# Kernel tuning notes

Hardware: AMD Instinct MI355X
Metric: run time of the kernel (lower is better)

The kernel has to match this reference:

```python
import jax, jax.numpy as jnp
import numpy as np

B, N, M = 16, 4096, 1024
IN_C, OUT_C, D = 6, 128, 64


def _gn(x, w, b, groups, eps=1e-5):
    # GroupNorm over (C//groups, L) per group; x: [B, C, L]
    Bb, C, L = x.shape
    xg = x.reshape(Bb, groups, C // groups, L)
    mu = xg.mean(axis=(2, 3), keepdims=True)
    var = xg.var(axis=(2, 3), keepdims=True)
    xn = ((xg - mu) * jax.lax.rsqrt(var + eps)).reshape(Bb, C, L)
    return xn * w[None, :, None] + b[None, :, None]


def _sa(xq, xkv, xyz_q, xyz_kv, qk_w, v_w, v_b, t_w, t_b, gn_w, gn_b, p_w, pg_w):
    # offset self-attention (PCT SA_Layer), q/k share weights
    pq = jnp.einsum('bcn,dc->bnd', xyz_q, p_w)              # [B,N,D]
    pk = jnp.einsum('bcm,dc->bdm', xyz_kv, pg_w)            # [B,D,M]
    q = jnp.einsum('bcn,dc->bnd', xq, qk_w) + pq            # [B,N,D]
    k = jnp.einsum('bcm,dc->bdm', xkv, qk_w) + pk           # [B,D,M]
    v = jnp.einsum('bcm,dc->bdm', xkv, v_w) + v_b[None, :, None] + pk
    attn = jax.nn.softmax(jnp.einsum('bnd,bdm->bnm', q, k), axis=-1)
    attn = attn / (1e-9 + attn.sum(axis=1, keepdims=True))  # L1 renorm over queries
    x_r = jnp.einsum('bnm,bdm->bnd', attn, v)               # [B,N,D]
    t = jnp.einsum('bnd,od->bon', q - x_r, t_w) + t_b[None, :, None]
    t = jax.nn.relu(_gn(t, gn_w, gn_b, 4))
    return jnp.swapaxes(q, 1, 2) + t                        # [B,D,N]


def _forward(x, x_global, xyz, xyz_global, conv1_w, gn1_w, gn1_b, conv2_w, gn2_w, gn2_b, sa_qk_w, sa_v_w, sa_v_b, sa_trans_w, sa_trans_b, sa_gn_w, sa_gn_b, sa_pos_w, sa_posG_w, fuse_w, fuse_gn_w, fuse_gn_b, convs1_w, convs1_b, gns1_w, gns1_b, convs2_w, convs2_b, gns2_w, gns2_b):
    h = jax.nn.relu(_gn(jnp.einsum('bcn,oc->bon', x, conv1_w), gn1_w, gn1_b, 16))
    hg = jax.nn.relu(_gn(jnp.einsum('bcm,oc->bom', x_global, conv2_w), gn2_w, gn2_b, 16))
    outs = []
    cur = h
    for i in range(4):
        cur = _sa(cur, hg, xyz, xyz_global, sa_qk_w[i], sa_v_w[i], sa_v_b[i],
                  sa_trans_w[i], sa_trans_b[i], sa_gn_w[i], sa_gn_b[i],
                  sa_pos_w[i], sa_posG_w[i])
        outs.append(cur)
    xc = jnp.concatenate(outs, axis=1)                      # [B,4D,N]
    xf = jax.nn.leaky_relu(_gn(jnp.einsum('bcn,oc->bon', xc, fuse_w), fuse_gn_w, fuse_gn_b, 16), 0.2)
    s1 = jax.nn.relu(_gn(jnp.einsum('bcn,oc->bon', xf, convs1_w) + convs1_b[None, :, None], gns1_w, gns1_b, 8))
    # dropout is identity in eval mode
    s2 = jax.nn.relu(_gn(jnp.einsum('bcn,oc->bon', s1, convs2_w) + convs2_b[None, :, None], gns2_w, gns2_b, 4))
    return jnp.swapaxes(s2, 1, 2)                           # [B,N,OUT_C]


def setup_inputs() -> dict:
    ks = jax.random.split(jax.random.key(0), 16)
    f = lambda k, s, sc=0.1: jax.random.normal(k, s, dtype=jnp.float32) * sc
    return {
        'x': f(ks[0], (B, IN_C, N), 1.0),
        'x_global': f(ks[1], (B, 32, M), 1.0),
        'xyz': f(ks[2], (B, 3, N), 1.0),
        'xyz_global': f(ks[3], (B, 3, M), 1.0),
        'conv1_w': f(ks[4], (D, IN_C)),
        'gn1_w': jnp.ones((D,), jnp.float32), 'gn1_b': jnp.zeros((D,), jnp.float32),
        'conv2_w': f(ks[5], (D, 32)),
        'gn2_w': jnp.ones((D,), jnp.float32), 'gn2_b': jnp.zeros((D,), jnp.float32),
        'sa_qk_w': f(ks[6], (4, D, D)),
        'sa_v_w': f(ks[7], (4, D, D)),
        'sa_v_b': jnp.zeros((4, D), jnp.float32),
        'sa_trans_w': f(ks[8], (4, D, D)),
        'sa_trans_b': jnp.zeros((4, D), jnp.float32),
        'sa_gn_w': jnp.ones((4, D), jnp.float32), 'sa_gn_b': jnp.zeros((4, D), jnp.float32),
        'sa_pos_w': f(ks[9], (4, D, 3)),
        'sa_posG_w': f(ks[10], (4, D, 3)),
        'fuse_w': f(ks[11], (2 * D, 4 * D)),
        'fuse_gn_w': jnp.ones((2 * D,), jnp.float32), 'fuse_gn_b': jnp.zeros((2 * D,), jnp.float32),
        'convs1_w': f(ks[12], (512, 2 * D)),
        'convs1_b': jnp.zeros((512,), jnp.float32),
        'gns1_w': jnp.ones((512,), jnp.float32), 'gns1_b': jnp.zeros((512,), jnp.float32),
        'convs2_w': f(ks[13], (OUT_C, 512)),
        'convs2_b': jnp.zeros((OUT_C,), jnp.float32),
        'gns2_w': jnp.ones((OUT_C,), jnp.float32), 'gns2_b': jnp.zeros((OUT_C,), jnp.float32),
    }


def reference(x, x_global, xyz, xyz_global, conv1_w, gn1_w, gn1_b, conv2_w, gn2_w, gn2_b, sa_qk_w, sa_v_w, sa_v_b, sa_trans_w, sa_trans_b, sa_gn_w, sa_gn_b, sa_pos_w, sa_posG_w, fuse_w, fuse_gn_w, fuse_gn_b, convs1_w, convs1_b, gns1_w, gns1_b, convs2_w, convs2_b, gns2_w, gns2_b):
    return _forward(x, x_global, xyz, xyz_global, conv1_w, gn1_w, gn1_b, conv2_w, gn2_w, gn2_b, sa_qk_w, sa_v_w, sa_v_b, sa_trans_w, sa_trans_b, sa_gn_w, sa_gn_b, sa_pos_w, sa_posG_w, fuse_w, fuse_gn_w, fuse_gn_b, convs1_w, convs1_b, gns1_w, gns1_b, convs2_w, convs2_b, gns2_w, gns2_b)
```

## Files before the change

### kernel.cpp

```cpp
#include <hip/hip_runtime.h>
#include <hip/hip_bf16.h>

namespace {

constexpr int BB = 16;
constexpr int NN = 4096;
constexpr int MM = 1024;

using f32x4  = __attribute__((ext_vector_type(4))) float;
using bf16x8 = __attribute__((ext_vector_type(8))) short;

__device__ __forceinline__ float actf(float x, int act) {
    if (act == 1) return fmaxf(x, 0.f);
    if (act == 2) return x >= 0.f ? x : 0.2f * x;
    return x;
}

__device__ __forceinline__ ushort f2bf(float x) {
    __hip_bfloat16 h = __float2bfloat16(x);
    return *reinterpret_cast<ushort*>(&h);
}

__device__ __forceinline__ uint hilo_pack(float x) {
    ushort h = f2bf(x);
    float hf = __uint_as_float(((uint)h) << 16);
    ushort l = f2bf(x - hf);
    return (uint)h | ((uint)l << 16);
}

__device__ __forceinline__ void split8(const uint* d, bf16x8& hi, bf16x8& lo) {
    union { uint u[4]; bf16x8 v; } H, L;
#pragma unroll
    for (int j = 0; j < 4; ++j) {
        H.u[j] = (d[2 * j] & 0xffffu) | (d[2 * j + 1] << 16);
        L.u[j] = (d[2 * j] >> 16) | (d[2 * j + 1] & 0xffff0000u);
    }
    hi = H.v; lo = L.v;
}

__global__ __launch_bounds__(256)
void conv_mfma(const float* __restrict__ X, int C, long x_bs,
               const float* __restrict__ W,
               const float* __restrict__ X2, long x2_bs,
               const float* __restrict__ W2,
               const float* __restrict__ bias,
               float* __restrict__ Y, long y_bs, int L)
{
    __shared__ uint Wp[64 * 33];
    __shared__ uint Xp[128 * 33];
    const int t  = threadIdx.x;
    const int b  = blockIdx.z;
    const int o0 = blockIdx.y * 64;
    const int l0 = blockIdx.x * 128;
    const int w  = t >> 6;
    const int ln = t & 15;
    const int lq = (t >> 4) & 3;
    const int wo = (w & 1) * 32;
    const int wl = (w >> 1) * 64;
    const int sl  = t & 127;
    const int sch = (t >> 7) * 16;

    f32x4 acc[2][4];
#pragma unroll
    for (int i = 0; i < 2; ++i)
#pragma unroll
        for (int j = 0; j < 4; ++j) acc[i][j] = (f32x4){0.f, 0.f, 0.f, 0.f};

    for (int c0 = 0; c0 < C; c0 += 32) {
        __syncthreads();
#pragma unroll
        for (int i = 0; i < 2; ++i) {
            int f = i * 256 + t;
            int r = f >> 3, q4 = (f & 7) * 4;
            float4 wv = *reinterpret_cast<const float4*>(&W[(long)(o0 + r) * C + c0 + q4]);
            Wp[r * 33 + q4 + 0] = hilo_pack(wv.x);
            Wp[r * 33 + q4 + 1] = hilo_pack(wv.y);
            Wp[r * 33 + q4 + 2] = hilo_pack(wv.z);
            Wp[r * 33 + q4 + 3] = hilo_pack(wv.w);
        }
        {
            const float* xc = X + (long)b * x_bs + (long)(c0 + sch) * L + l0 + sl;
            uint tmp[16];
#pragma unroll
            for (int c = 0; c < 16; ++c) tmp[c] = hilo_pack(xc[(long)c * L]);
#pragma unroll
            for (int c4 = 0; c4 < 4; ++c4) {
                uint4 v = make_uint4(tmp[c4 * 4], tmp[c4 * 4 + 1],
                                     tmp[c4 * 4 + 2], tmp[c4 * 4 + 3]);
                *reinterpret_cast<uint4*>(&Xp[sl * 33 + sch + c4 * 4]) = v;
            }
        }
        __syncthreads();

        bf16x8 ahi[2], alo[2];
#pragma unroll
        for (int ot = 0; ot < 2; ++ot) {
            uint d[8];
            *reinterpret_cast<uint4*>(d) =
                *reinterpret_cast<const uint4*>(&Wp[(wo + ot * 16 + ln) * 33 + lq * 8]);
            *reinterpret_cast<uint4*>(d + 4) =
                *reinterpret_cast<const uint4*>(&Wp[(wo + ot * 16 + ln) * 33 + lq * 8 + 4]);
            split8(d, ahi[ot], alo[ot]);
        }
#pragma unroll
        for (int lt = 0; lt < 4; ++lt) {
            uint d[8];
            *reinterpret_cast<uint4*>(d) =
                *reinterpret_cast<const uint4*>(&Xp[(wl + lt * 16 + ln) * 33 + lq * 8]);
            *reinterpret_cast<uint4*>(d + 4) =
                *reinterpret_cast<const uint4*>(&Xp[(wl + lt * 16 + ln) * 33 + lq * 8 + 4]);
            bf16x8 bhi, blo;
            split8(d, bhi, blo);
#pragma unroll
            for (int ot = 0; ot < 2; ++ot) {
                acc[ot][lt] = __builtin_amdgcn_mfma_f32_16x16x32_bf16(alo[ot], bhi, acc[ot][lt], 0, 0, 0);
                acc[ot][lt] = __builtin_amdgcn_mfma_f32_16x16x32_bf16(ahi[ot], blo, acc[ot][lt], 0, 0, 0);
                acc[ot][lt] = __builtin_amdgcn_mfma_f32_16x16x32_bf16(ahi[ot], bhi, acc[ot][lt], 0, 0, 0);
            }
        }
    }

    float x2v[4][3];
    if (X2) {
#pragma unroll
        for (int lt = 0; lt < 4; ++lt) {
            const int l = l0 + wl + lt * 16 + ln;
#pragma unroll
            for (int c = 0; c < 3; ++c)
                x2v[lt][c] = X2[(long)b * x2_bs + (long)c * L + l];
        }
    }
#pragma unroll
    for (int ot = 0; ot < 2; ++ot)
#pragma unroll
        for (int r = 0; r < 4; ++r) {
            const int o = o0 + wo + ot * 16 + lq * 4 + r;
            float base = bias ? bias[o] : 0.f;
            float w20 = 0.f, w21 = 0.f, w22 = 0.f;
            if (X2) {
                w20 = W2[o * 3 + 0];
                w21 = W2[o * 3 + 1];
                w22 = W2[o * 3 + 2];
            }
#pragma unroll
            for (int lt = 0; lt < 4; ++lt) {
                const int l = l0 + wl + lt * 16 + ln;
                float val = acc[ot][lt][r] + base;
                if (X2)
                    val += w20 * x2v[lt][0] + w21 * x2v[lt][1] + w22 * x2v[lt][2];
                Y[(long)b * y_bs + (long)o * L + l] = val;
            }
        }
}

__global__ __launch_bounds__(256)
void conv_gemm(const float* __restrict__ X1, int C1, long x1_bs,
               const float* __restrict__ W1,
               const float* __restrict__ X2, int C2, long x2_bs,
               const float* __restrict__ W2,
               const float* __restrict__ bias,
               float* __restrict__ Y, long y_bs, int L)
{
    __shared__ float Wt[64][17];
    __shared__ float Xt[16][128];
    const int t  = threadIdx.x;
    const int b  = blockIdx.z;
    const int o0 = blockIdx.y * 64;
    const int l0 = blockIdx.x * 128;
    const int ty = t >> 4, tx = t & 15;

    float acc[4][8];
#pragma unroll
    for (int i = 0; i < 4; ++i)
#pragma unroll
        for (int j = 0; j < 8; ++j) acc[i][j] = 0.f;

    for (int pass = 0; pass < 2; ++pass) {
        const float* X = pass ? X2 : X1;
        const float* W = pass ? W2 : W1;
        const int    C = pass ? C2 : C1;
        const long xbs = pass ? x2_bs : x1_bs;
        if (C <= 0 || X == nullptr) continue;
        for (int c0 = 0; c0 < C; c0 += 16) {
            __syncthreads();
#pragma unroll
            for (int i = 0; i < 4; ++i) {
                int flat = i * 256 + t;
                int oo = flat >> 4, kk = flat & 15;
                Wt[oo][kk] = (c0 + kk < C) ? W[(long)(o0 + oo) * C + c0 + kk] : 0.f;
            }
#pragma unroll
            for (int i = 0; i < 2; ++i) {
                int f4 = i * 256 + t;
                int kk = f4 >> 5, c4 = f4 & 31;
                float4 xv = make_float4(0.f, 0.f, 0.f, 0.f);
                if (c0 + kk < C)
                    xv = *reinterpret_cast<const float4*>(
                        X + (long)b * xbs + (long)(c0 + kk) * L + l0 + c4 * 4);
                *reinterpret_cast<float4*>(&Xt[kk][c4 * 4]) = xv;
            }
            __syncthreads();
#pragma unroll
            for (int kk = 0; kk < 16; ++kk) {
                float wv[4];
#pragma unroll
                for (int i = 0; i < 4; ++i) wv[i] = Wt[ty * 4 + i][kk];
                float4 xa = *reinterpret_cast<const float4*>(&Xt[kk][tx * 8]);
                float4 xb = *reinterpret_cast<const float4*>(&Xt[kk][tx * 8 + 4]);
                float xv[8] = {xa.x, xa.y, xa.z, xa.w, xb.x, xb.y, xb.z, xb.w};
#pragma unroll
                for (int i = 0; i < 4; ++i)
#pragma unroll
                    for (int j = 0; j < 8; ++j) acc[i][j] += wv[i] * xv[j];
            }
        }
    }

#pragma unroll
    for (int i = 0; i < 4; ++i) {
        const int oo = o0 + ty * 4 + i;
        const float bv = bias ? bias[oo] : 0.f;
        float* yp = Y + (long)b * y_bs + (long)oo * L + l0 + tx * 8;
        float4 v0 = make_float4(acc[i][0] + bv, acc[i][1] + bv, acc[i][2] + bv, acc[i][3] + bv);
        float4 v1 = make_float4(acc[i][4] + bv, acc[i][5] + bv, acc[i][6] + bv, acc[i][7] + bv);
        *reinterpret_cast<float4*>(yp)     = v0;
        *reinterpret_cast<float4*>(yp + 4) = v1;
    }
}

__global__ __launch_bounds__(256)
void gn_stats(const float* __restrict__ Y, long y_bs, int cpg, int L, int G,
              float* __restrict__ stats)
{
    const int bg = blockIdx.x;
    const int b = bg / G, g = bg - b * G;
    const float* p = Y + (long)b * y_bs + (long)g * cpg * L;
    const long cnt = (long)cpg * L;
    float s = 0.f, ss = 0.f;
    for (long i = (long)threadIdx.x * 4; i < cnt; i += 256 * 4) {
        float4 v = *reinterpret_cast<const float4*>(p + i);
        s  += v.x + v.y + v.z + v.w;
        ss += v.x * v.x + v.y * v.y + v.z * v.z + v.w * v.w;
    }
    __shared__ float rs[256], rss[256];
    rs[threadIdx.x] = s; rss[threadIdx.x] = ss;
    __syncthreads();
    for (int st = 128; st > 0; st >>= 1) {
        if (threadIdx.x < st) {
            rs[threadIdx.x]  += rs[threadIdx.x + st];
            rss[threadIdx.x] += rss[threadIdx.x + st];
        }
        __syncthreads();
    }
    if (threadIdx.x == 0) {
        float mu  = rs[0] / (float)cnt;
        float var = rss[0] / (float)cnt - mu * mu;
        stats[bg * 2]     = mu;
        stats[bg * 2 + 1] = rsqrtf(var + 1e-5f);
    }
}

__global__ __launch_bounds__(256)
void gn_apply(const float* __restrict__ src, long s_bs,
              float* __restrict__ dst, long d_bs,
              const float* __restrict__ res, long r_bs,
              const float* __restrict__ w, const float* __restrict__ bb,
              const float* __restrict__ stats,
              int C, int cpg, int L, int act)
{
    const long total4 = (long)BB * C * L / 4;
    const int G = C / cpg;
    for (long i4 = (long)blockIdx.x * 256 + threadIdx.x; i4 < total4;
         i4 += (long)gridDim.x * 256) {
        long flat = i4 * 4;
        int b = (int)(flat / ((long)C * L));
        long rem = flat - (long)b * C * L;
        int c = (int)(rem / L);
        long li = rem - (long)c * L;
        int sidx = (b * G + c / cpg) * 2;
        float mu = stats[sidx], rsig = stats[sidx + 1];
        float sc = rsig * w[c];
        float sh = bb[c] - mu * sc;
        float4 vv = *reinterpret_cast<const float4*>(src + (long)b * s_bs + (long)c * L + li);
        float4 ov;
        ov.x = actf(vv.x * sc + sh, act);
        ov.y = actf(vv.y * sc + sh, act);
        ov.z = actf(vv.z * sc + sh, act);
        ov.w = actf(vv.w * sc + sh, act);
        if (res) {
            float4 rv = *reinterpret_cast<const float4*>(res + (long)b * r_bs + (long)c * L + li);
            ov.x += rv.x; ov.y += rv.y; ov.z += rv.z; ov.w += rv.w;
        }
        *reinterpret_cast<float4*>(dst + (long)b * d_bs + (long)c * L + li) = ov;
    }
}

__global__ __launch_bounds__(256)
void tcvt(const float* __restrict__ in, ushort* __restrict__ out, int L)
{
    __shared__ float ls[64][65];
    const int t = threadIdx.x, b = blockIdx.y;
    const int l0 = blockIdx.x * 64;
#pragma unroll
    for (int i = 0; i < 16; ++i) {
        int f = i * 256 + t;
        int d = f >> 6, l = f & 63;
        ls[d][l] = in[(long)b * 64 * L + (long)d * L + l0 + l];
    }
    __syncthreads();
#pragma unroll
    for (int i = 0; i < 16; ++i) {
        int f = i * 256 + t;
        int l = f >> 6, d = f & 63;
        out[((long)b * L + l0 + l) * 64 + d] = f2bf(ls[d][l]);
    }
}

__global__ __launch_bounds__(256)
void attn_stats_mfma(const ushort* __restrict__ qt, const ushort* __restrict__ kt,
                     float* __restrict__ rowmax, float* __restrict__ rowinv,
                     float* __restrict__ csp)
{
    __shared__ float red[16][5];
    __shared__ float rs_mx[16], rs_inv[16];

    const int t  = threadIdx.x;
    const int b  = blockIdx.y;
    const int n0 = blockIdx.x * 16;
    const int w  = t >> 6;
    const int ln = t & 15;
    const int lq = (t >> 4) & 3;

    const ushort* qtb = qt + ((long)b * NN + n0) * 64;
    const ushort* ktb = kt + (long)b * MM * 64;

    bf16x8 aq[2];
#pragma unroll
    for (int ks = 0; ks < 2; ++ks)
        aq[ks] = *reinterpret_cast<const bf16x8*>(qtb + (long)ln * 64 + ks * 32 + lq * 8);

    f32x4 sc[16];
#pragma unroll
    for (int i = 0; i < 16; ++i) {
        const int m0 = (w * 16 + i) * 16;
        f32x4 acc = {0.f, 0.f, 0.f, 0.f};
#pragma unroll
        for (int ks = 0; ks < 2; ++ks) {
            bf16x8 bk = *reinterpret_cast<const bf16x8*>(
                ktb + (long)(m0 + ln) * 64 + ks * 32 + lq * 8);
            acc = __builtin_amdgcn_mfma_f32_16x16x32_bf16(aq[ks], bk, acc, 0, 0, 0);
        }
        sc[i] = acc;
    }

    float m4[4];
#pragma unroll
    for (int r = 0; r < 4; ++r) {
        float mx = sc[0][r];
#pragma unroll
        for (int i = 1; i < 16; ++i) mx = fmaxf(mx, sc[i][r]);
#pragma unroll
        for (int off = 1; off <= 8; off <<= 1) mx = fmaxf(mx, __shfl_xor(mx, off, 64));
        m4[r] = mx;
    }
    if (ln == 0)
#pragma unroll
        for (int r = 0; r < 4; ++r) red[lq * 4 + r][w] = m4[r];
    __syncthreads();
    if (t < 16) {
        float mx = fmaxf(fmaxf(red[t][0], red[t][1]), fmaxf(red[t][2], red[t][3]));
        rs_mx[t] = mx;
        rowmax[(long)b * NN + n0 + t] = mx;
    }
    __syncthreads();

    float mxr[4], s4[4];
#pragma unroll
    for (int r = 0; r < 4; ++r) { mxr[r] = rs_mx[lq * 4 + r]; s4[r] = 0.f; }
#pragma unroll
    for (int i = 0; i < 16; ++i)
#pragma unroll
        for (int r = 0; r < 4; ++r) {
            float e = __expf(sc[i][r] - mxr[r]);
            sc[i][r] = e;
            s4[r] += e;
        }
#pragma unroll
    for (int r = 0; r < 4; ++r)
#pragma unroll
        for (int off = 1; off <= 8; off <<= 1) s4[r] += __shfl_xor(s4[r], off, 64);
    if (ln == 0)
#pragma unroll
        for (int r = 0; r < 4; ++r) red[lq * 4 + r][w] = s4[r];
    __syncthreads();
    if (t < 16) {
        float es = red[t][0] + red[t][1] + red[t][2] + red[t][3];
        float inv = 1.0f / es;
        rs_inv[t] = inv;
        rowinv[(long)b * NN + n0 + t] = inv;
    }
    __syncthreads();

    float riv[4];
#pragma unroll
    for (int r = 0; r < 4; ++r) riv[r] = rs_inv[lq * 4 + r];
    const long cbase = ((long)b * (NN / 16) + blockIdx.x) * MM;
#pragma unroll
    for (int i = 0; i < 16; ++i) {
        float c = sc[i][0] * riv[0] + sc[i][1] * riv[1] + sc[i][2] * riv[2] + sc[i][3] * riv[3];
        c += __shfl_xor(c, 16, 64);
        c += __shfl_xor(c, 32, 64);
        if (lq == 0) csp[cbase + (w * 16 + i) * 16 + ln] = c;
    }
}

__global__ __launch_bounds__(256)
void attn_pv_mfma(const ushort* __restrict__ qt, const ushort* __restrict__ kt,
                  const ushort* __restrict__ vb,
                  const float* __restrict__ rowmax, const float* __restrict__ rowinv,
                  const float* __restrict__ qg, float* __restrict__ ug)
{
    __shared__ ushort Pb[16 * 1024];

    const int t  = threadIdx.x;
    const int b  = blockIdx.y;
    const int n0 = blockIdx.x * 16;
    const int w  = t >> 6;
    const int ln = t & 15;
    const int lq = (t >> 4) & 3;

    const ushort* qtb = qt + ((long)b * NN + n0) * 64;
    const ushort* ktb = kt + (long)b * MM * 64;

    float mx[4], ri[4];
#pragma unroll
    for (int r = 0; r < 4; ++r) {
        mx[r] = rowmax[(long)b * NN + n0 + lq * 4 + r];
        ri[r] = rowinv[(long)b * NN + n0 + lq * 4 + r];
    }

    bf16x8 aq[2];
#pragma unroll
    for (int ks = 0; ks < 2; ++ks)
        aq[ks] = *reinterpret_cast<const bf16x8*>(qtb + (long)ln * 64 + ks * 32 + lq * 8);

#pragma unroll
    for (int i = 0; i < 16; ++i) {
        const int m0 = (w * 16 + i) * 16;
        f32x4 acc = {0.f, 0.f, 0.f, 0.f};
#pragma unroll
        for (int ks = 0; ks < 2; ++ks) {
            bf16x8 bk = *reinterpret_cast<const bf16x8*>(
                ktb + (long)(m0 + ln) * 64 + ks * 32 + lq * 8);
            acc = __builtin_amdgcn_mfma_f32_16x16x32_bf16(aq[ks], bk, acc, 0, 0, 0);
        }
#pragma unroll
        for (int r = 0; r < 4; ++r) {
            const int n = lq * 4 + r;
            float p = __expf(acc[r] - mx[r]) * ri[r];
            Pb[n * 1024 + ((m0 + ln) ^ ((n & 7) << 3))] = f2bf(p);
        }
    }
    __syncthreads();

    const ushort* vbb = vb + (long)b * 64 * MM;
    const int d0 = w * 16;
    f32x4 acc = {0.f, 0.f, 0.f, 0.f};
#pragma unroll 8
    for (int ks = 0; ks < 32; ++ks) {
        bf16x8 av = *reinterpret_cast<const bf16x8*>(
            vbb + (long)(d0 + ln) * MM + ks * 32 + lq * 8);
        bf16x8 bp = *reinterpret_cast<const bf16x8*>(
            &Pb[ln * 1024 + ((ks * 32 + lq * 8) ^ ((ln & 7) << 3))]);
        acc = __builtin_amdgcn_mfma_f32_16x16x32_bf16(av, bp, acc, 0, 0, 0);
    }

    const long qb = (long)b * 64 * NN;
#pragma unroll
    for (int r = 0; r < 4; ++r) {
        const int dd = d0 + lq * 4 + r;
        const long idx = qb + (long)dd * NN + n0 + ln;
        ug[idx] = qg[idx] - acc[r];
    }
}

__global__ __launch_bounds__(256)
void colsum_reduce(const float* __restrict__ csp, float* __restrict__ cs, int NT)
{
    int idx = blockIdx.x * 256 + threadIdx.x;
    int b = idx / MM, m = idx - b * MM;
    const float* p = csp + (long)b * NT * MM + m;
    float s = 0.f;
    for (int i = 0; i < NT; ++i) s += p[(long)i * MM];
    cs[idx] = s;
}

__global__ __launch_bounds__(256)
void vscale_cvt(const float* __restrict__ v, const float* __restrict__ cs,
                ushort* __restrict__ vb)
{
    long i4 = (long)blockIdx.x * 256 + threadIdx.x;
    long flat = i4 * 4;
    int b = (int)(flat / (64L * MM));
    int m = (int)(flat % MM);
    float4 vv = *reinterpret_cast<const float4*>(v + flat);
    float4 cv = *reinterpret_cast<const float4*>(cs + (long)b * MM + m);
    ushort4 o;
    o.x = f2bf(vv.x / (1e-9f + cv.x));
    o.y = f2bf(vv.y / (1e-9f + cv.y));
    o.z = f2bf(vv.z / (1e-9f + cv.z));
    o.w = f2bf(vv.w / (1e-9f + cv.w));
    *reinterpret_cast<ushort4*>(vb + flat) = o;
}

__global__ __launch_bounds__(256)
void gn_out_transpose(const float* __restrict__ s2,
                      const float* __restrict__ w, const float* __restrict__ bb,
                      const float* __restrict__ stats,
                      float* __restrict__ out)
{
    __shared__ float ls[128 * 65];
    const int t = threadIdx.x;
    const int b = blockIdx.y;
    const int n0 = blockIdx.x * 64;
#pragma unroll
    for (int i = 0; i < 8; ++i) {
        int f4 = i * 256 + t;
        int o = f4 >> 4, c4 = f4 & 15;
        float4 vv = *reinterpret_cast<const float4*>(
            s2 + (long)b * 128 * NN + (long)o * NN + n0 + c4 * 4);
        int sidx = (b * 4 + (o >> 5)) * 2;
        float mu = stats[sidx], rsig = stats[sidx + 1];
        float sc = rsig * w[o], sh = bb[o] - mu * sc;
        ls[o * 65 + c4 * 4 + 0] = fmaxf(vv.x * sc + sh, 0.f);
        ls[o * 65 + c4 * 4 + 1] = fmaxf(vv.y * sc + sh, 0.f);
        ls[o * 65 + c4 * 4 + 2] = fmaxf(vv.z * sc + sh, 0.f);
        ls[o * 65 + c4 * 4 + 3] = fmaxf(vv.w * sc + sh, 0.f);
    }
    __syncthreads();
#pragma unroll
    for (int i = 0; i < 8; ++i) {
        int f4 = i * 256 + t;
        int nn = f4 >> 5, o4 = f4 & 31;
        float4 ov;
        ov.x = ls[(o4 * 4 + 0) * 65 + nn];
        ov.y = ls[(o4 * 4 + 1) * 65 + nn];
        ov.z = ls[(o4 * 4 + 2) * 65 + nn];
        ov.w = ls[(o4 * 4 + 3) * 65 + nn];
        *reinterpret_cast<float4*>(out + (long)b * NN * 128 + (long)(n0 + nn) * 128 + o4 * 4) = ov;
    }
}

}

extern "C" void kernel_launch(void* const* d_in, const int* in_sizes, int n_in,
                              void* d_out, int out_size, void* d_ws, size_t ws_size,
                              hipStream_t stream)
{
    (void)in_sizes; (void)n_in; (void)out_size; (void)ws_size;

    const float* x         = (const float*)d_in[0];
    const float* x_global  = (const float*)d_in[1];
    const float* xyz       = (const float*)d_in[2];
    const float* xyz_g     = (const float*)d_in[3];
    const float* conv1_w   = (const float*)d_in[4];
    const float* gn1_w     = (const float*)d_in[5];
    const float* gn1_b     = (const float*)d_in[6];
    const float* conv2_w   = (const float*)d_in[7];
    const float* gn2_w     = (const float*)d_in[8];
    const float* gn2_b     = (const float*)d_in[9];
    const float* sa_qk_w   = (const float*)d_in[10];
    const float* sa_v_w    = (const float*)d_in[11];
    const float* sa_v_b    = (const float*)d_in[12];
    const float* sa_t_w    = (const float*)d_in[13];
    const float* sa_t_b    = (const float*)d_in[14];
    const float* sa_gn_w   = (const float*)d_in[15];
    const float* sa_gn_b   = (const float*)d_in[16];
    const float* sa_pos_w  = (const float*)d_in[17];
    const float* sa_posG_w = (const float*)d_in[18];
    const float* fuse_w    = (const float*)d_in[19];
    const float* fuse_gn_w = (const float*)d_in[20];
    const float* fuse_gn_b = (const float*)d_in[21];
    const float* convs1_w  = (const float*)d_in[22];
    const float* convs1_b  = (const float*)d_in[23];
    const float* gns1_w    = (const float*)d_in[24];
    const float* gns1_b    = (const float*)d_in[25];
    const float* convs2_w  = (const float*)d_in[26];
    const float* convs2_b  = (const float*)d_in[27];
    const float* gns2_w    = (const float*)d_in[28];
    const float* gns2_b    = (const float*)d_in[29];

    constexpr long SZ_BN  = (long)BB * 64 * NN;
    constexpr long SZ_BM  = (long)BB * 64 * MM;
    constexpr long SZ_CSP = (long)BB * (NN / 16) * MM;

    float* ws = (float*)d_ws;
    long o = 0;
    float* p_h   = ws + o; o += SZ_BN;
    float* p_hg  = ws + o; o += SZ_BM;
    float* p_q   = ws + o; o += SZ_BN;
    float* p_k   = ws + o; o += SZ_BM;
    float* p_v   = ws + o; o += SZ_BM;
    float* p_u   = ws + o; o += SZ_BN;
    float* p_csp = ws + o; o += SZ_CSP;
    float* p_cs  = ws + o; o += (long)BB * MM;
    float* p_xc  = ws + o; o += (long)BB * 256 * NN;
    float* p_xf  = ws + o; o += (long)BB * 128 * NN;
    float* p_st  = ws + o; o += 4096;
    float* p_rmx = ws + o; o += (long)BB * NN;
    float* p_rin = ws + o; o += (long)BB * NN;
    float* p_s1  = ws;
    float* p_s2  = p_xf;
    ushort* p_qt = (ushort*)p_xf;
    ushort* p_kt = (ushort*)(p_xf + 2097152);
    ushort* p_vb = (ushort*)(p_xf + 2097152 + 524288);

    conv_gemm<<<dim3(NN / 128, 1, BB), 256, 0, stream>>>(
        x, 6, 6L * NN, conv1_w, nullptr, 0, 0, nullptr, nullptr, p_h, 64L * NN, NN);
    gn_stats<<<BB * 16, 256, 0, stream>>>(p_h, 64L * NN, 4, NN, 16, p_st);
    gn_apply<<<2048, 256, 0, stream>>>(p_h, 64L * NN, p_h, 64L * NN, nullptr, 0,
                                       gn1_w, gn1_b, p_st, 64, 4, NN, 1);
    conv_mfma<<<dim3(MM / 128, 1, BB), 256, 0, stream>>>(
        x_global, 32, 32L * MM, conv2_w, nullptr, 0, nullptr, nullptr, p_hg, 64L * MM, MM);
    gn_stats<<<BB * 16, 256, 0, stream>>>(p_hg, 64L * MM, 4, MM, 16, p_st);
    gn_apply<<<2048, 256, 0, stream>>>(p_hg, 64L * MM, p_hg, 64L * MM, nullptr, 0,
                                       gn2_w, gn2_b, p_st, 64, 4, MM, 1);

    const float* cur = p_h;
    long cur_bs = 64L * NN;
    for (int i = 0; i < 4; ++i) {
        conv_mfma<<<dim3(NN / 128, 1, BB), 256, 0, stream>>>(
            cur, 64, cur_bs, sa_qk_w + i * 4096,
            xyz, 3L * NN, sa_pos_w + i * 192, nullptr, p_q, 64L * NN, NN);
        tcvt<<<dim3(NN / 64, BB), 256, 0, stream>>>(p_q, p_qt, NN);
        conv_mfma<<<dim3(MM / 128, 1, BB), 256, 0, stream>>>(
            p_hg, 64, 64L * MM, sa_qk_w + i * 4096,
            xyz_g, 3L * MM, sa_posG_w + i * 192, nullptr, p_k, 64L * MM, MM);
        tcvt<<<dim3(MM / 64, BB), 256, 0, stream>>>(p_k, p_kt, MM);
        conv_mfma<<<dim3(MM / 128, 1, BB), 256, 0, stream>>>(
            p_hg, 64, 64L * MM, sa_v_w + i * 4096,
            xyz_g, 3L * MM, sa_posG_w + i * 192, sa_v_b + i * 64, p_v, 64L * MM, MM);
        attn_stats_mfma<<<dim3(NN / 16, BB), 256, 0, stream>>>(p_qt, p_kt, p_rmx, p_rin, p_csp);
        colsum_reduce<<<BB * MM / 256, 256, 0, stream>>>(p_csp, p_cs, NN / 16);
        vscale_cvt<<<BB * 64 * MM / 1024, 256, 0, stream>>>(p_v, p_cs, p_vb);
        attn_pv_mfma<<<dim3(NN / 16, BB), 256, 0, stream>>>(
            p_qt, p_kt, p_vb, p_rmx, p_rin, p_q, p_u);
        conv_mfma<<<dim3(NN / 128, 1, BB), 256, 0, stream>>>(
            p_u, 64, 64L * NN, sa_t_w + i * 4096,
            nullptr, 0, nullptr, sa_t_b + i * 64, p_h, 64L * NN, NN);
        gn_stats<<<BB * 4, 256, 0, stream>>>(p_h, 64L * NN, 16, NN, 4, p_st);
        gn_apply<<<2048, 256, 0, stream>>>(p_h, 64L * NN,
                                           p_xc + (long)i * 64 * NN, 256L * NN,
                                           p_q, 64L * NN,
                                           sa_gn_w + i * 64, sa_gn_b + i * 64, p_st,
                                           64, 16, NN, 1);
        cur = p_xc + (long)i * 64 * NN;
        cur_bs = 256L * NN;
    }

    conv_mfma<<<dim3(NN / 128, 2, BB), 256, 0, stream>>>(
        p_xc, 256, 256L * NN, fuse_w, nullptr, 0, nullptr, nullptr, p_xf, 128L * NN, NN);
    gn_stats<<<BB * 16, 256, 0, stream>>>(p_xf, 128L * NN, 8, NN, 16, p_st);
    gn_apply<<<2048, 256, 0, stream>>>(p_xf, 128L * NN, p_xf, 128L * NN, nullptr, 0,
                                       fuse_gn_w, fuse_gn_b, p_st, 128, 8, NN, 2);
    conv_mfma<<<dim3(NN / 128, 8, BB), 256, 0, stream>>>(
        p_xf, 128, 128L * NN, convs1_w, nullptr, 0, nullptr, convs1_b, p_s1, 512L * NN, NN);
    gn_stats<<<BB * 8, 256, 0, stream>>>(p_s1, 512L * NN, 64, NN, 8, p_st);
    gn_apply<<<2048, 256, 0, stream>>>(p_s1, 512L * NN, p_s1, 512L * NN, nullptr, 0,
                                       gns1_w, gns1_b, p_st, 512, 64, NN, 1);
    conv_mfma<<<dim3(NN / 128, 2, BB), 256, 0, stream>>>(
        p_s1, 512, 512L * NN, convs2_w, nullptr, 0, nullptr, convs2_b, p_s2, 128L * NN, NN);
    gn_stats<<<BB * 4, 256, 0, stream>>>(p_s2, 128L * NN, 32, NN, 4, p_st);
    gn_out_transpose<<<dim3(NN / 64, BB), 256, 0, stream>>>(
        p_s2, gns2_w, gns2_b, p_st, (float*)d_out);
}
```

Measured before the change: 1.697 ms.

## Tile attention PV kernel over 32 queries with chunked double-buffered P

The P·V attention kernel now handles 32 query rows per block instead of 16. It processes the key dimension in four 256-wide chunks, writing the probabilities into a double-buffered LDS tile and accumulating two output tiles per wave, so each V fragment load serves twice as many queries. In both the stats and PV kernels, K fragment loads are grouped ahead of their MFMAs so more loads are in flight. The goal is to cut V and K global traffic and overlap exp/P generation with the PV MFMAs. The cost is fewer blocks, more registers per thread and a barrier per chunk.

```diff
diff --git a/kernel.cpp b/kernel.cpp
--- a/kernel.cpp
+++ b/kernel.cpp
@@ -341,16 +341,23 @@
 
     f32x4 sc[16];
 #pragma unroll
-    for (int i = 0; i < 16; ++i) {
-        const int m0 = (w * 16 + i) * 16;
-        f32x4 acc = {0.f, 0.f, 0.f, 0.f};
-#pragma unroll
-        for (int ks = 0; ks < 2; ++ks) {
-            bf16x8 bk = *reinterpret_cast<const bf16x8*>(
-                ktb + (long)(m0 + ln) * 64 + ks * 32 + lq * 8);
-            acc = __builtin_amdgcn_mfma_f32_16x16x32_bf16(aq[ks], bk, acc, 0, 0, 0);
-        }
-        sc[i] = acc;
+    for (int ib = 0; ib < 4; ++ib) {
+        bf16x8 bk[4][2];
+#pragma unroll
+        for (int ii = 0; ii < 4; ++ii) {
+            const int m0 = (w * 16 + ib * 4 + ii) * 16;
+#pragma unroll
+            for (int ks = 0; ks < 2; ++ks)
+                bk[ii][ks] = *reinterpret_cast<const bf16x8*>(
+                    ktb + (long)(m0 + ln) * 64 + ks * 32 + lq * 8);
+        }
+#pragma unroll
+        for (int ii = 0; ii < 4; ++ii) {
+            f32x4 acc = {0.f, 0.f, 0.f, 0.f};
+            acc = __builtin_amdgcn_mfma_f32_16x16x32_bf16(aq[0], bk[ii][0], acc, 0, 0, 0);
+            acc = __builtin_amdgcn_mfma_f32_16x16x32_bf16(aq[1], bk[ii][1], acc, 0, 0, 0);
+            sc[ib * 4 + ii] = acc;
+        }
     }
 
     float m4[4];
@@ -420,23 +427,27 @@
                   const float* __restrict__ rowmax, const float* __restrict__ rowinv,
                   const float* __restrict__ qg, float* __restrict__ ug)
 {
-    __shared__ ushort Pb[16 * 1024];
+    __shared__ ushort Pb[2][32 * 256];
 
     const int t  = threadIdx.x;
     const int b  = blockIdx.y;
-    const int n0 = blockIdx.x * 16;
+    const int n0 = blockIdx.x * 32;
     const int w  = t >> 6;
+    const int rt = w & 1;
+    const int ms = w >> 1;
     const int ln = t & 15;
     const int lq = (t >> 4) & 3;
-
-    const ushort* qtb = qt + ((long)b * NN + n0) * 64;
+    const int d0 = w * 16;
+
+    const ushort* qtb = qt + ((long)b * NN + n0 + rt * 16) * 64;
     const ushort* ktb = kt + (long)b * MM * 64;
+    const ushort* vbb = vb + (long)b * 64 * MM;
 
     float mx[4], ri[4];
 #pragma unroll
     for (int r = 0; r < 4; ++r) {
-        mx[r] = rowmax[(long)b * NN + n0 + lq * 4 + r];
-        ri[r] = rowinv[(long)b * NN + n0 + lq * 4 + r];
+        mx[r] = rowmax[(long)b * NN + n0 + rt * 16 + lq * 4 + r];
+        ri[r] = rowinv[(long)b * NN + n0 + rt * 16 + lq * 4 + r];
     }
 
     bf16x8 aq[2];
@@ -444,44 +455,60 @@
     for (int ks = 0; ks < 2; ++ks)
         aq[ks] = *reinterpret_cast<const bf16x8*>(qtb + (long)ln * 64 + ks * 32 + lq * 8);
 
-#pragma unroll
-    for (int i = 0; i < 16; ++i) {
-        const int m0 = (w * 16 + i) * 16;
-        f32x4 acc = {0.f, 0.f, 0.f, 0.f};
-#pragma unroll
-        for (int ks = 0; ks < 2; ++ks) {
-            bf16x8 bk = *reinterpret_cast<const bf16x8*>(
-                ktb + (long)(m0 + ln) * 64 + ks * 32 + lq * 8);
-            acc = __builtin_amdgcn_mfma_f32_16x16x32_bf16(aq[ks], bk, acc, 0, 0, 0);
-        }
+    f32x4 acc2[2];
+    acc2[0] = (f32x4){0.f, 0.f, 0.f, 0.f};
+    acc2[1] = (f32x4){0.f, 0.f, 0.f, 0.f};
+
+    const int swz = (ln & 7) << 3;
+
+    for (int c = 0; c < 4; ++c) {
+        bf16x8 bk[8][2];
+#pragma unroll
+        for (int it = 0; it < 8; ++it) {
+            const int m = c * 256 + ms * 128 + it * 16 + ln;
+#pragma unroll
+            for (int ks = 0; ks < 2; ++ks)
+                bk[it][ks] = *reinterpret_cast<const bf16x8*>(
+                    ktb + (long)m * 64 + ks * 32 + lq * 8);
+        }
+        ushort* pc = &Pb[c & 1][0];
+#pragma unroll
+        for (int it = 0; it < 8; ++it) {
+            f32x4 acc = {0.f, 0.f, 0.f, 0.f};
+            acc = __builtin_amdgcn_mfma_f32_16x16x32_bf16(aq[0], bk[it][0], acc, 0, 0, 0);
+            acc = __builtin_amdgcn_mfma_f32_16x16x32_bf16(aq[1], bk[it][1], acc, 0, 0, 0);
+            const int mc = ms * 128 + it * 16 + ln;
+#pragma unroll
+            for (int r = 0; r < 4; ++r) {
+                const int n = rt * 16 + lq * 4 + r;
+                float p = __expf(acc[r] - mx[r]) * ri[r];
+                pc[n * 256 + (mc ^ ((n & 7) << 3))] = f2bf(p);
+            }
+        }
+        __syncthreads();
+#pragma unroll
+        for (int ks = 0; ks < 8; ++ks) {
+            bf16x8 av = *reinterpret_cast<const bf16x8*>(
+                vbb + (long)(d0 + ln) * MM + c * 256 + ks * 32 + lq * 8);
+            const int mo = ks * 32 + lq * 8;
+#pragma unroll
+            for (int nt = 0; nt < 2; ++nt) {
+                bf16x8 bp = *reinterpret_cast<const bf16x8*>(
+                    &pc[(nt * 16 + ln) * 256 + (mo ^ swz)]);
+                acc2[nt] = __builtin_amdgcn_mfma_f32_16x16x32_bf16(av, bp, acc2[nt], 0, 0, 0);
+            }
+        }
+    }
+
+    const long qb = (long)b * 64 * NN;
+#pragma unroll
+    for (int nt = 0; nt < 2; ++nt)
 #pragma unroll
         for (int r = 0; r < 4; ++r) {
-            const int n = lq * 4 + r;
-            float p = __expf(acc[r] - mx[r]) * ri[r];
-            Pb[n * 1024 + ((m0 + ln) ^ ((n & 7) << 3))] = f2bf(p);
-        }
-    }
-    __syncthreads();
-
-    const ushort* vbb = vb + (long)b * 64 * MM;
-    const int d0 = w * 16;
-    f32x4 acc = {0.f, 0.f, 0.f, 0.f};
-#pragma unroll 8
-    for (int ks = 0; ks < 32; ++ks) {
-        bf16x8 av = *reinterpret_cast<const bf16x8*>(
-            vbb + (long)(d0 + ln) * MM + ks * 32 + lq * 8);
-        bf16x8 bp = *reinterpret_cast<const bf16x8*>(
-            &Pb[ln * 1024 + ((ks * 32 + lq * 8) ^ ((ln & 7) << 3))]);
-        acc = __builtin_amdgcn_mfma_f32_16x16x32_bf16(av, bp, acc, 0, 0, 0);
-    }
-
-    const long qb = (long)b * 64 * NN;
-#pragma unroll
-    for (int r = 0; r < 4; ++r) {
-        const int dd = d0 + lq * 4 + r;
-        const long idx = qb + (long)dd * NN + n0 + ln;
-        ug[idx] = qg[idx] - acc[r];
-    }
+            const int dd = d0 + lq * 4 + r;
+            const long idx = qb + (long)dd * NN + n0 + nt * 16 + ln;
+            ug[idx] = qg[idx] - acc2[nt][r];
+        }
 }
 
 __global__ __launch_bounds__(256)
@@ -643,7 +670,7 @@
         attn_stats_mfma<<<dim3(NN / 16, BB), 256, 0, stream>>>(p_qt, p_kt, p_rmx, p_rin, p_csp);
         colsum_reduce<<<BB * MM / 256, 256, 0, stream>>>(p_csp, p_cs, NN / 16);
         vscale_cvt<<<BB * 64 * MM / 1024, 256, 0, stream>>>(p_v, p_cs, p_vb);
-        attn_pv_mfma<<<dim3(NN / 16, BB), 256, 0, stream>>>(
+        attn_pv_mfma<<<dim3(NN / 32, BB), 256, 0, stream>>>(
             p_qt, p_kt, p_vb, p_rmx, p_rin, p_q, p_u);
         conv_mfma<<<dim3(NN / 128, 1, BB), 256, 0, stream>>>(
             p_u, 64, 64L * NN, sa_t_w + i * 4096,
```

Measured after the change: 1.582 ms, median of 2. -6.8%, faster.
